# Performance work log

Measured on AMD Instinct MI355X. Metric: run time of the kernel, lower is better.

Reference implementation:

```python
import jax, jax.numpy as jnp
import numpy as np

B, NX, NY, NZ, C = 4, 432, 496, 1, 64
PT, PS = 4096, 16384  # pillars per sample (template / search)


def _make_coords(key, P):
    # unique (y, x) cells per batch element -> no duplicate scatter indices
    flat = jax.vmap(lambda k: jax.random.permutation(k, NY * NX)[:P])(
        jax.random.split(key, B))  # [B, P]
    y = flat // NX
    x = flat % NX
    b = jnp.repeat(jnp.arange(B), P)
    z = jnp.zeros_like(b)
    return jnp.stack([b, z, y.reshape(-1), x.reshape(-1)], axis=1).astype(jnp.int32)


def setup_inputs() -> dict:
    key = jax.random.key(0)
    k1, k2, k3, k4 = jax.random.split(key, 4)
    return {
        "template_voxel_features": jax.random.normal(k1, (B * PT, C), dtype=jnp.float32),
        "template_voxel_coords": _make_coords(k2, PT),
        "search_voxel_features": jax.random.normal(k3, (B * PS, C), dtype=jnp.float32),
        "search_voxel_coords": _make_coords(k4, PS),
    }


def _scatter_bev(feats, coords):
    # coords: [N, 4] = (batch, z, y, x); index = z + y*nx + x (nz == 1)
    idx = coords[:, 1] + coords[:, 2] * NX + coords[:, 3]
    gidx = coords[:, 0] * (NY * NX) + idx  # global flat index over batch*grid
    grid = jnp.zeros((B * NY * NX, feats.shape[1]), dtype=feats.dtype)
    grid = grid.at[gidx].set(feats)
    # [B, ny, nx, C] -> [B, C*nz, ny, nx]
    return grid.reshape(B, NY, NX, feats.shape[1]).transpose(0, 3, 1, 2)


def reference(template_voxel_features, template_voxel_coords,
              search_voxel_features, search_voxel_coords):
    t_spatial = _scatter_bev(template_voxel_features, template_voxel_coords)
    x_spatial = _scatter_bev(search_voxel_features, search_voxel_coords)
    return t_spatial, x_spatial
```

## Files before the change

kernel.cpp:

```cpp
#include <hip/hip_runtime.h>

constexpr int Bv  = 4;
constexpr int NXv = 432;
constexpr int NYv = 496;
constexpr int Cv  = 64;
constexpr int PLANE = NYv * NXv;
constexpr int GRID_CELLS = Bv * PLANE;
constexpr int PER_TENSOR_T4 = GRID_CELLS / 4;

typedef float v4f __attribute__((ext_vector_type(4)));

__global__ void build_all_kernel(const int* __restrict__ t_coords, int nt,
                                 const int* __restrict__ s_coords, int ns,
                                 int* __restrict__ map) {
    int i = blockIdx.x * blockDim.x + threadIdx.x;
    if (i < nt) {
        const int4 c = reinterpret_cast<const int4*>(t_coords)[i];
        map[(c.x * NYv + c.z) * NXv + c.w] = i + 1;
    } else if (i < nt + ns) {
        int j = i - nt;
        const int4 c = reinterpret_cast<const int4*>(s_coords)[j];
        map[GRID_CELLS + (c.x * NYv + c.z) * NXv + c.w] = j + 1;
    }
}

__global__ __launch_bounds__(256) void gather_all_kernel(
        const int* __restrict__ map,
        const float* __restrict__ t_feats,
        const float* __restrict__ s_feats,
        const float* __restrict__ zero_row,
        float* __restrict__ out, size_t half) {
    int tid = blockIdx.x * blockDim.x + threadIdx.x;
    const int which = (tid >= PER_TENSOR_T4) ? 1 : 0;
    const int lid = tid - which * PER_TENSOR_T4;

    const int*   mp    = map + which * GRID_CELLS;
    const float* feats = which ? s_feats : t_feats;
    float*       obase = out + (which ? half : 0);

    const int g = lid * 4;
    const int b = lid / (PLANE / 4);

    const int4 m = *reinterpret_cast<const int4*>(mp + g);

    const float* p0 = (m.x > 0) ? feats + (size_t)(m.x - 1) * Cv : zero_row;
    const float* p1 = (m.y > 0) ? feats + (size_t)(m.y - 1) * Cv : zero_row;
    const float* p2 = (m.z > 0) ? feats + (size_t)(m.z - 1) * Cv : zero_row;
    const float* p3 = (m.w > 0) ? feats + (size_t)(m.w - 1) * Cv : zero_row;

    float* o = obase + g + (size_t)b * (Cv - 1) * PLANE;

    for (int ch = 0; ch < 4; ++ch) {
        v4f r0[4], r1[4], r2[4], r3[4];
        const int cb = ch * 16;
        #pragma unroll
        for (int j = 0; j < 4; ++j) {
            r0[j] = *reinterpret_cast<const v4f*>(p0 + cb + j * 4);
            r1[j] = *reinterpret_cast<const v4f*>(p1 + cb + j * 4);
            r2[j] = *reinterpret_cast<const v4f*>(p2 + cb + j * 4);
            r3[j] = *reinterpret_cast<const v4f*>(p3 + cb + j * 4);
        }
        #pragma unroll
        for (int j = 0; j < 4; ++j) {
            const v4f s0 = {r0[j].x, r1[j].x, r2[j].x, r3[j].x};
            const v4f s1 = {r0[j].y, r1[j].y, r2[j].y, r3[j].y};
            const v4f s2 = {r0[j].z, r1[j].z, r2[j].z, r3[j].z};
            const v4f s3 = {r0[j].w, r1[j].w, r2[j].w, r3[j].w};
            __builtin_nontemporal_store(s0, reinterpret_cast<v4f*>(o + (size_t)(cb + j * 4 + 0) * PLANE));
            __builtin_nontemporal_store(s1, reinterpret_cast<v4f*>(o + (size_t)(cb + j * 4 + 1) * PLANE));
            __builtin_nontemporal_store(s2, reinterpret_cast<v4f*>(o + (size_t)(cb + j * 4 + 2) * PLANE));
            __builtin_nontemporal_store(s3, reinterpret_cast<v4f*>(o + (size_t)(cb + j * 4 + 3) * PLANE));
        }
    }
}

__global__ void direct_scatter_kernel(const float* __restrict__ feats,
                                      const int* __restrict__ coords, int n,
                                      float* __restrict__ out) {
    int i = blockIdx.x * blockDim.x + threadIdx.x;
    if (i >= n * Cv) return;
    int v = i >> 6;
    int c = i & 63;
    int b = coords[v * 4 + 0];
    int y = coords[v * 4 + 2];
    int x = coords[v * 4 + 3];
    out[((size_t)(b * Cv + c) * NYv + y) * NXv + x] = feats[(size_t)v * Cv + c];
}

extern "C" void kernel_launch(void* const* d_in, const int* in_sizes, int n_in,
                              void* d_out, int out_size, void* d_ws, size_t ws_size,
                              hipStream_t stream) {
    const float* t_feats  = (const float*)d_in[0];
    const int*   t_coords = (const int*)d_in[1];
    const float* s_feats  = (const float*)d_in[2];
    const int*   s_coords = (const int*)d_in[3];
    float* out = (float*)d_out;

    const int NT = in_sizes[0] / Cv;
    const int NS = in_sizes[2] / Cv;
    const size_t half = (size_t)out_size / 2;

    const size_t map_bytes = 2ull * GRID_CELLS * sizeof(int);
    const size_t ws_need   = map_bytes + 256;

    if (ws_size >= ws_need) {
        int* map = (int*)d_ws;
        const float* zero_row = (const float*)((char*)d_ws + map_bytes);

        (void)hipMemsetAsync(d_ws, 0, ws_need, stream);

        build_all_kernel<<<(NT + NS + 255) / 256, 256, 0, stream>>>(
            t_coords, NT, s_coords, NS, map);

        const int gthreads = 2 * PER_TENSOR_T4;
        gather_all_kernel<<<gthreads / 256, 256, 0, stream>>>(
            map, t_feats, s_feats, zero_row, out, half);
    } else {
        (void)hipMemsetAsync(d_out, 0, (size_t)out_size * sizeof(float), stream);
        direct_scatter_kernel<<<(NT * Cv + 255) / 256, 256, 0, stream>>>(
            t_feats, t_coords, NT, out);
        direct_scatter_kernel<<<(NS * Cv + 255) / 256, 256, 0, stream>>>(
            s_feats, s_coords, NS, out + half);
    }
}
```

Baseline: 93.66 us.

## Fuse memset, map build and gather into one cooperative persistent kernel

Replaces the memset plus two kernel launches with a single cooperative kernel. It zeroes the index map, builds it, then gathers into the output, with grid-wide syncs between phases and a grid-stride loop over the gather work. This removes the launch and inter-kernel gaps, but adds two grid.sync barriers and caps the grid at occupancy-limited persistent blocks, which may reduce latency hiding in the bandwidth-bound gather. The non-workspace fallback path is removed, and the launcher now returns without writing output when the workspace is too small.

```diff
diff --git a/kernel.cpp b/kernel.cpp
--- a/kernel.cpp
+++ b/kernel.cpp
@@ -1,4 +1,7 @@
 #include <hip/hip_runtime.h>
+#include <hip/hip_cooperative_groups.h>
+
+namespace cg = cooperative_groups;
 
 constexpr int Bv  = 4;
 constexpr int NXv = 432;
@@ -7,8 +10,93 @@
 constexpr int PLANE = NYv * NXv;
 constexpr int GRID_CELLS = Bv * PLANE;
 constexpr int PER_TENSOR_T4 = GRID_CELLS / 4;
+constexpr int GATHER_ITEMS  = 2 * PER_TENSOR_T4;
+constexpr int FULL_BLOCKS   = GATHER_ITEMS / 256;
+constexpr int ZTOT4 = (2 * GRID_CELLS + Cv) / 4;
 
 typedef float v4f __attribute__((ext_vector_type(4)));
+
+__device__ __forceinline__ void gather_item(
+        int it, const int* __restrict__ map,
+        const float* __restrict__ t_feats, const float* __restrict__ s_feats,
+        const float* __restrict__ zero_row, float* __restrict__ out, size_t half) {
+    const int which = (it >= PER_TENSOR_T4) ? 1 : 0;
+    const int lid = it - which * PER_TENSOR_T4;
+
+    const int*   mp    = map + which * GRID_CELLS;
+    const float* feats = which ? s_feats : t_feats;
+    float*       obase = out + (which ? half : 0);
+
+    const int g = lid * 4;
+    const int b = lid / (PLANE / 4);
+
+    const int4 m = *reinterpret_cast<const int4*>(mp + g);
+
+    const float* p0 = (m.x > 0) ? feats + (size_t)(m.x - 1) * Cv : zero_row;
+    const float* p1 = (m.y > 0) ? feats + (size_t)(m.y - 1) * Cv : zero_row;
+    const float* p2 = (m.z > 0) ? feats + (size_t)(m.z - 1) * Cv : zero_row;
+    const float* p3 = (m.w > 0) ? feats + (size_t)(m.w - 1) * Cv : zero_row;
+
+    float* o = obase + g + (size_t)b * (Cv - 1) * PLANE;
+
+    for (int ch = 0; ch < 4; ++ch) {
+        const int cb = ch * 16;
+        v4f r0[4], r1[4], r2[4], r3[4];
+        #pragma unroll
+        for (int j = 0; j < 4; ++j) {
+            r0[j] = *reinterpret_cast<const v4f*>(p0 + cb + j * 4);
+            r1[j] = *reinterpret_cast<const v4f*>(p1 + cb + j * 4);
+            r2[j] = *reinterpret_cast<const v4f*>(p2 + cb + j * 4);
+            r3[j] = *reinterpret_cast<const v4f*>(p3 + cb + j * 4);
+        }
+        #pragma unroll
+        for (int j = 0; j < 4; ++j) {
+            const v4f s0 = {r0[j].x, r1[j].x, r2[j].x, r3[j].x};
+            const v4f s1 = {r0[j].y, r1[j].y, r2[j].y, r3[j].y};
+            const v4f s2 = {r0[j].z, r1[j].z, r2[j].z, r3[j].z};
+            const v4f s3 = {r0[j].w, r1[j].w, r2[j].w, r3[j].w};
+            __builtin_nontemporal_store(s0, reinterpret_cast<v4f*>(o + (size_t)(cb + j * 4 + 0) * PLANE));
+            __builtin_nontemporal_store(s1, reinterpret_cast<v4f*>(o + (size_t)(cb + j * 4 + 1) * PLANE));
+            __builtin_nontemporal_store(s2, reinterpret_cast<v4f*>(o + (size_t)(cb + j * 4 + 2) * PLANE));
+            __builtin_nontemporal_store(s3, reinterpret_cast<v4f*>(o + (size_t)(cb + j * 4 + 3) * PLANE));
+        }
+    }
+}
+
+__global__ __launch_bounds__(256) void fused_all_kernel(
+        const int* __restrict__ t_coords, int nt,
+        const int* __restrict__ s_coords, int ns,
+        const float* __restrict__ t_feats,
+        const float* __restrict__ s_feats,
+        int* __restrict__ map,
+        float* __restrict__ out, size_t half) {
+    cg::grid_group grid = cg::this_grid();
+    const int nth = gridDim.x * blockDim.x;
+    const int tid = blockIdx.x * blockDim.x + threadIdx.x;
+
+    {
+        const int4 z = {0, 0, 0, 0};
+        int4* m4 = reinterpret_cast<int4*>(map);
+        for (int i = tid; i < ZTOT4; i += nth) m4[i] = z;
+    }
+    grid.sync();
+
+    for (int i = tid; i < nt + ns; i += nth) {
+        if (i < nt) {
+            const int4 c = reinterpret_cast<const int4*>(t_coords)[i];
+            map[(c.x * NYv + c.z) * NXv + c.w] = i + 1;
+        } else {
+            const int j = i - nt;
+            const int4 c = reinterpret_cast<const int4*>(s_coords)[j];
+            map[GRID_CELLS + (c.x * NYv + c.z) * NXv + c.w] = j + 1;
+        }
+    }
+    grid.sync();
+
+    const float* zero_row = reinterpret_cast<const float*>(map + 2 * GRID_CELLS);
+    for (int it = tid; it < GATHER_ITEMS; it += nth)
+        gather_item(it, map, t_feats, s_feats, zero_row, out, half);
+}
 
 __global__ void build_all_kernel(const int* __restrict__ t_coords, int nt,
                                  const int* __restrict__ s_coords, int ns,
@@ -31,60 +119,7 @@
         const float* __restrict__ zero_row,
         float* __restrict__ out, size_t half) {
     int tid = blockIdx.x * blockDim.x + threadIdx.x;
-    const int which = (tid >= PER_TENSOR_T4) ? 1 : 0;
-    const int lid = tid - which * PER_TENSOR_T4;
-
-    const int*   mp    = map + which * GRID_CELLS;
-    const float* feats = which ? s_feats : t_feats;
-    float*       obase = out + (which ? half : 0);
-
-    const int g = lid * 4;
-    const int b = lid / (PLANE / 4);
-
-    const int4 m = *reinterpret_cast<const int4*>(mp + g);
-
-    const float* p0 = (m.x > 0) ? feats + (size_t)(m.x - 1) * Cv : zero_row;
-    const float* p1 = (m.y > 0) ? feats + (size_t)(m.y - 1) * Cv : zero_row;
-    const float* p2 = (m.z > 0) ? feats + (size_t)(m.z - 1) * Cv : zero_row;
-    const float* p3 = (m.w > 0) ? feats + (size_t)(m.w - 1) * Cv : zero_row;
-
-    float* o = obase + g + (size_t)b * (Cv - 1) * PLANE;
-
-    for (int ch = 0; ch < 4; ++ch) {
-        v4f r0[4], r1[4], r2[4], r3[4];
-        const int cb = ch * 16;
-        #pragma unroll
-        for (int j = 0; j < 4; ++j) {
-            r0[j] = *reinterpret_cast<const v4f*>(p0 + cb + j * 4);
-            r1[j] = *reinterpret_cast<const v4f*>(p1 + cb + j * 4);
-            r2[j] = *reinterpret_cast<const v4f*>(p2 + cb + j * 4);
-            r3[j] = *reinterpret_cast<const v4f*>(p3 + cb + j * 4);
-        }
-        #pragma unroll
-        for (int j = 0; j < 4; ++j) {
-            const v4f s0 = {r0[j].x, r1[j].x, r2[j].x, r3[j].x};
-            const v4f s1 = {r0[j].y, r1[j].y, r2[j].y, r3[j].y};
-            const v4f s2 = {r0[j].z, r1[j].z, r2[j].z, r3[j].z};
-            const v4f s3 = {r0[j].w, r1[j].w, r2[j].w, r3[j].w};
-            __builtin_nontemporal_store(s0, reinterpret_cast<v4f*>(o + (size_t)(cb + j * 4 + 0) * PLANE));
-            __builtin_nontemporal_store(s1, reinterpret_cast<v4f*>(o + (size_t)(cb + j * 4 + 1) * PLANE));
-            __builtin_nontemporal_store(s2, reinterpret_cast<v4f*>(o + (size_t)(cb + j * 4 + 2) * PLANE));
-            __builtin_nontemporal_store(s3, reinterpret_cast<v4f*>(o + (size_t)(cb + j * 4 + 3) * PLANE));
-        }
-    }
-}
-
-__global__ void direct_scatter_kernel(const float* __restrict__ feats,
-                                      const int* __restrict__ coords, int n,
-                                      float* __restrict__ out) {
-    int i = blockIdx.x * blockDim.x + threadIdx.x;
-    if (i >= n * Cv) return;
-    int v = i >> 6;
-    int c = i & 63;
-    int b = coords[v * 4 + 0];
-    int y = coords[v * 4 + 2];
-    int x = coords[v * 4 + 3];
-    out[((size_t)(b * Cv + c) * NYv + y) * NXv + x] = feats[(size_t)v * Cv + c];
+    gather_item(tid, map, t_feats, s_feats, zero_row, out, half);
 }
 
 extern "C" void kernel_launch(void* const* d_in, const int* in_sizes, int n_in,
@@ -96,30 +131,38 @@
     const int*   s_coords = (const int*)d_in[3];
     float* out = (float*)d_out;
 
-    const int NT = in_sizes[0] / Cv;
-    const int NS = in_sizes[2] / Cv;
-    const size_t half = (size_t)out_size / 2;
+    int NT = in_sizes[0] / Cv;
+    int NS = in_sizes[2] / Cv;
+    size_t half = (size_t)out_size / 2;
 
     const size_t map_bytes = 2ull * GRID_CELLS * sizeof(int);
     const size_t ws_need   = map_bytes + 256;
 
-    if (ws_size >= ws_need) {
-        int* map = (int*)d_ws;
-        const float* zero_row = (const float*)((char*)d_ws + map_bytes);
+    if (ws_size < ws_need) return;
 
+    int* map = (int*)d_ws;
+    const float* zero_row = (const float*)((char*)d_ws + map_bytes);
+
+    int perCU = 0;
+    hipError_t qe = hipOccupancyMaxActiveBlocksPerMultiprocessor(
+        &perCU, reinterpret_cast<const void*>(fused_all_kernel), 256, 0);
+
+    bool coop_done = false;
+    if (qe == hipSuccess && perCU > 0) {
+        int blocks = perCU * 256;
+        if (blocks > FULL_BLOCKS) blocks = FULL_BLOCKS;
+        void* args[] = {&t_coords, &NT, &s_coords, &NS,
+                        &t_feats, &s_feats, &map, &out, &half};
+        hipError_t le = hipLaunchCooperativeKernel(
+            (const void*)fused_all_kernel, dim3(blocks), dim3(256), args, 0, stream);
+        coop_done = (le == hipSuccess);
+    }
+
+    if (!coop_done) {
         (void)hipMemsetAsync(d_ws, 0, ws_need, stream);
-
         build_all_kernel<<<(NT + NS + 255) / 256, 256, 0, stream>>>(
             t_coords, NT, s_coords, NS, map);
-
-        const int gthreads = 2 * PER_TENSOR_T4;
-        gather_all_kernel<<<gthreads / 256, 256, 0, stream>>>(
+        gather_all_kernel<<<FULL_BLOCKS, 256, 0, stream>>>(
             map, t_feats, s_feats, zero_row, out, half);
-    } else {
-        (void)hipMemsetAsync(d_out, 0, (size_t)out_size * sizeof(float), stream);
-        direct_scatter_kernel<<<(NT * Cv + 255) / 256, 256, 0, stream>>>(
-            t_feats, t_coords, NT, out);
-        direct_scatter_kernel<<<(NS * Cv + 255) / 256, 256, 0, stream>>>(
-            s_feats, s_coords, NS, out + half);
     }
 }
```

New measurement: 198.2 us. 2.12x slower.
